# Performance work log

Measured on AMD Instinct MI355X. Metric: run time of the kernel, lower is better.

Reference implementation:

```python
import jax, jax.numpy as jnp
import numpy as np
import math

N_HEAD = 12

def alibi_slopes(h):
    x = (2 ** 8) ** (1.0 / h)
    return jnp.array([1.0 / x ** (i + 1) for i in range(h)], dtype=jnp.float32)

def setup_inputs() -> dict:
    key = jax.random.key(0)
    k0, k1, k2 = jax.random.split(key, 3)
    B, T, C = 4, 2048, 576
    x = jax.random.normal(k0, (B, T, C), dtype=jnp.float32)
    w_qkv = jax.random.normal(k1, (3 * C, C), dtype=jnp.float32) * 0.02
    w_proj = jax.random.normal(k2, (C, C), dtype=jnp.float32) * 0.02
    return {"x": x, "w_qkv": w_qkv, "w_proj": w_proj}

def reference(x, w_qkv, w_proj):
    B, T, C = x.shape
    H = N_HEAD
    D = C // H
    qkv = x @ w_qkv.T  # [B,T,3C]
    q, k, v = jnp.split(qkv, 3, axis=2)
    q = q.reshape(B, T, H, D).transpose(0, 2, 1, 3)  # [B,H,T,D]
    k = k.reshape(B, T, H, D).transpose(0, 2, 1, 3)
    v = v.reshape(B, T, H, D).transpose(0, 2, 1, 3)
    # value residual with v1=None: v = 0.5*v + 0.5*v = v (faithful no-op)
    scale = 1.0 / math.sqrt(D)
    att = jnp.einsum('bhid,bhjd->bhij', q, k) * scale  # [B,H,T,T]
    # ALiBi bias as written: (col - row).clamp(min=0) * slope (zero on causal part)
    col = jnp.arange(T, dtype=jnp.float32)[None, :]
    row = jnp.arange(T, dtype=jnp.float32)[:, None]
    bias = jnp.maximum(col - row, 0.0)[None, :, :] * alibi_slopes(H)[:, None, None]  # [H,T,T]
    att = att + bias[None]
    causal = (jnp.arange(T)[None, :] <= jnp.arange(T)[:, None])  # [T,T] lower-tri
    att = jnp.where(causal[None, None], att, -jnp.inf)
    att = jax.nn.softmax(att, axis=-1)
    y = jnp.einsum('bhij,bhjd->bhid', att, v)  # [B,H,T,D]
    y = y.transpose(0, 2, 1, 3).reshape(B, T, C)
    return y @ w_proj.T
```

## Files before the change

### kernel.cpp

```cpp
#include <hip/hip_runtime.h>
#include <math.h>

#define Bn 4
#define Tn 2048
#define Cn 576
#define Hn 12
#define Dn 48
#define Mn (Bn*Tn)
#define NPAD 1792

#define QSCALE (1.4426950408889634f * 0.14433756729740643f)

typedef short  short8  __attribute__((ext_vector_type(8)));
typedef float  floatx4 __attribute__((ext_vector_type(4)));
typedef unsigned short ushort_t;
typedef unsigned short ushort8_t __attribute__((ext_vector_type(8)));

static __device__ __forceinline__ unsigned short f2bf(float f) {
    union { float f; unsigned int u; } v; v.f = f;
    unsigned int r = v.u + 0x7FFFu + ((v.u >> 16) & 1u);
    return (unsigned short)(r >> 16);
}

static __device__ __forceinline__ unsigned int pack_trunc(float a, float b) {
    union { float f; unsigned int u; } ua, ub; ua.f = a; ub.f = b;
    return (ua.u >> 16) | (ub.u & 0xFFFF0000u);
}

static __device__ __forceinline__ void gload16(void* lds, const void* g) {
    __builtin_amdgcn_global_load_lds(
        (const __attribute__((address_space(1))) void*)g,
        (__attribute__((address_space(3))) void*)lds, 16, 0, 0);
}

template<int N> static __device__ __forceinline__ void vmgate() {
    if constexpr (N == 0)      asm volatile("s_waitcnt vmcnt(0)" ::: "memory");
    else if constexpr (N == 4) asm volatile("s_waitcnt vmcnt(4)" ::: "memory");
    else if constexpr (N == 8) asm volatile("s_waitcnt vmcnt(8)" ::: "memory");
}
static __device__ __forceinline__ void lgk0() {
    asm volatile("s_waitcnt lgkmcnt(0)" ::: "memory");
}
static __device__ __forceinline__ void barrier_fence() {
    asm volatile("" ::: "memory");
    __builtin_amdgcn_s_barrier();
    asm volatile("" ::: "memory");
}

template<int N> static __device__ __forceinline__ void wait_vm_lg() {
    if constexpr (N == 0)
        asm volatile("s_waitcnt vmcnt(0) lgkmcnt(0)" ::: "memory");
    else if constexpr (N == 3)
        asm volatile("s_waitcnt vmcnt(3) lgkmcnt(0)" ::: "memory");
    else if constexpr (N == 6)
        asm volatile("s_waitcnt vmcnt(6) lgkmcnt(0)" ::: "memory");
    else
        static_assert(N == -12345, "unsupported waitcnt immediate");
}

__global__ __launch_bounds__(256)
void cast3(const float* __restrict__ a, ushort_t* __restrict__ oa, int na4,
           const float* __restrict__ b, ushort_t* __restrict__ ob, int nb4,
           const float* __restrict__ c, ushort_t* __restrict__ oc, int nc4)
{
    int i = blockIdx.x * 256 + threadIdx.x;
    const float* src; ushort_t* dst; int idx;
    if (i < na4)                  { src = a; dst = oa; idx = i; }
    else if (i < na4 + nb4)       { src = b; dst = ob; idx = i - na4; }
    else if (i < na4 + nb4 + nc4) { src = c; dst = oc; idx = i - na4 - nb4; }
    else return;
    float4 v = ((const float4*)src)[idx];
    ushort4 o;
    o.x = f2bf(v.x); o.y = f2bf(v.y); o.z = f2bf(v.z); o.w = f2bf(v.w);
    ((ushort4*)dst)[idx] = o;
}

__global__ __launch_bounds__(512)
void gemm_qkv(const ushort_t* __restrict__ A, const ushort_t* __restrict__ W,
              ushort_t* __restrict__ outb)
{
    __shared__ __align__(16) ushort_t Ls[8][8192];

    const int tid  = threadIdx.x;
    const int wave = tid >> 6;
    const int lane = tid & 63;
    const int m    = lane & 15;
    const int g    = lane >> 4;
    const int wr   = wave >> 2;
    const int wn   = wave & 3;

    const int bid  = blockIdx.x;
    const int xcd  = bid & 7;
    const int slot = bid >> 3;
    const int ng   = slot % 7;
    const int mg   = xcd + 8 * (slot / 7);
    const int m0   = mg * 256;
    const int n0g  = ng * 256;

    const int srow = lane >> 2;
    const int schk = (lane & 3) * 16;
    const char* aS0 = (const char*)A + (size_t)(m0  + (wave*2+0)*16 + srow) * (Cn*2) + schk;
    const char* aS1 = (const char*)A + (size_t)(m0  + (wave*2+1)*16 + srow) * (Cn*2) + schk;
    const char* bS0 = (const char*)W + (size_t)(n0g + (wave*2+0)*16 + srow) * (Cn*2) + schk;
    const char* bS1 = (const char*)W + (size_t)(n0g + (wave*2+1)*16 + srow) * (Cn*2) + schk;

    const int aoff = (wr * 128 + m) * 64 + g * 16;
    const int boff = (wn * 64  + m) * 64 + g * 16;

    floatx4 acc[8][4];
    #pragma unroll
    for (int i = 0; i < 8; ++i)
        #pragma unroll
        for (int j = 0; j < 4; ++j)
            acc[i][j] = (floatx4){0.f, 0.f, 0.f, 0.f};

    short8 af[8], bf01[2], bf23[2];

    auto stageA = [&](int s) {
        gload16(&Ls[s][(wave*2+0)*512], aS0); aS0 += 64;
        gload16(&Ls[s][(wave*2+1)*512], aS1); aS1 += 64;
    };
    auto stageB = [&](int s) {
        gload16(&Ls[s][(wave*2+0)*512], bS0); bS0 += 64;
        gload16(&Ls[s][(wave*2+1)*512], bS1); bS1 += 64;
    };
    auto loadA = [&](int s) {
        const char* base = (const char*)&Ls[s][0] + aoff;
        #pragma unroll
        for (int mf = 0; mf < 8; ++mf) af[mf] = *(const short8*)(base + mf * 1024);
    };
    auto loadB = [&](int s, int nf0, short8 (&bf)[2]) {
        const char* base = (const char*)&Ls[s][0] + boff;
        bf[0] = *(const short8*)(base + (nf0 + 0) * 1024);
        bf[1] = *(const short8*)(base + (nf0 + 1) * 1024);
    };
    auto mfma16 = [&](short8 (&bf)[2], int nf0) {
        __builtin_amdgcn_s_setprio(1);
        #pragma unroll
        for (int mf = 0; mf < 8; ++mf) {
            acc[mf][nf0]     = __builtin_amdgcn_mfma_f32_16x16x32_bf16(af[mf], bf[0], acc[mf][nf0],     0, 0, 0);
            acc[mf][nf0 + 1] = __builtin_amdgcn_mfma_f32_16x16x32_bf16(af[mf], bf[1], acc[mf][nf0 + 1], 0, 0, 0);
        }
        __builtin_amdgcn_s_setprio(0);
    };

    stageA(0); stageB(1); stageA(2); stageB(3); stageA(4); stageB(5);
    vmgate<8>();
    barrier_fence();

    #define QKV_TILE(s0, d0, d1, d2, d3, G1m, G3m) do {                         \
        constexpr int A0 = (s0) & 7,      B0 = ((s0)+1) & 7;                    \
        constexpr int A1 = ((s0)+2) & 7,  B1 = ((s0)+3) & 7;                    \
        constexpr int S0 = ((s0)+6) & 7,  S1 = ((s0)+7) & 7;                    \
        constexpr int S2 = ((s0)+8) & 7,  S3 = ((s0)+9) & 7;                    \
                                                    \
        loadA(A0); loadB(B0, 0, bf01);                                          \
        if (d0) stageA(S0);                                                     \
        barrier_fence(); lgk0();                                                \
        mfma16(bf01, 0);                                                        \
        barrier_fence();                                                        \
                                                            \
        loadB(B0, 2, bf23);                                                     \
        if (d1) stageB(S1);                                                     \
        barrier_fence(); lgk0();                                                \
        mfma16(bf23, 2);                                                        \
        vmgate<G1m>();                                                          \
        barrier_fence();                                                        \
                                                    \
        loadA(A1); loadB(B1, 0, bf01);                                          \
        if (d2) stageA(S2);                                                     \
        barrier_fence(); lgk0();                                                \
        mfma16(bf01, 0);                                                        \
        barrier_fence();                                                        \
                                                            \
        loadB(B1, 2, bf23);                                                     \
        if (d3) stageB(S3);                                                     \
        barrier_fence(); lgk0();                                                \
        mfma16(bf23, 2);                                                        \
        vmgate<G3m>();                                                          \
        barrier_fence();                                                        \
    } while (0)

    #pragma unroll 1
    for (int tt = 0; tt < 3; ++tt) {
        QKV_TILE(0, 1, 1, 1, 1, 8, 8);
        QKV_TILE(4, 1, 1, 1, 1, 8, 8);
    }
    QKV_TILE(0, 1, 1, 1, 1, 8, 8);
    QKV_TILE(4, 1, 1, 0, 0, 8, 4);
    QKV_TILE(0, 0, 0, 0, 0, 0, -1);
    #undef QKV_TILE

    const size_t per = (size_t)Bn * Hn * Tn * Dn;
    const int b  = m0 >> 11;
    const int t0 = m0 & 2047;
    ushort_t* Lc = (ushort_t*)&Ls[0][0];

    #pragma unroll
    for (int h2 = 0; h2 < 2; ++h2) {
        const int  nbase = n0g + h2 * 128;
        const bool vmode = (nbase >= 1152);
        if ((wn >> 1) == h2) {
            if (!vmode) {
                #pragma unroll
                for (int mf = 0; mf < 8; ++mf)
                    #pragma unroll
                    for (int nf = 0; nf < 4; ++nf) {
                        const int  nfb = n0g + wn * 64 + nf * 16;
                        const float sc = (nfb < 576) ? QSCALE : 1.0f;
                        const int col = (wn & 1) * 64 + nf * 16 + m;
                        const int rb  = wr * 128 + mf * 16 + g * 4;
                        #pragma unroll
                        for (int r = 0; r < 4; ++r)
                            Lc[(rb + r) * 136 + col] = f2bf(acc[mf][nf][r] * sc);
                    }
            } else {
                #pragma unroll
                for (int mf = 0; mf < 8; ++mf)
                    #pragma unroll
                    for (int nf = 0; nf < 4; ++nf) {
                        const int col = (wn & 1) * 64 + nf * 16 + m;
                        const int rb  = wr * 128 + mf * 16 + g * 4;
                        ushort4 pk;
                        pk.x = f2bf(acc[mf][nf][0]); pk.y = f2bf(acc[mf][nf][1]);
                        pk.z = f2bf(acc[mf][nf][2]); pk.w = f2bf(acc[mf][nf][3]);
                        *(ushort4*)&Lc[col * 264 + rb] = pk;
                    }
            }
        }
        __syncthreads();
        if (!vmode) {
            #pragma unroll
            for (int it = 0; it < 8; ++it) {
                const int c   = tid + it * 512;
                const int row = c >> 4;
                const int c8  = (c & 15) * 8;
                const int n   = nbase + c8;
                const int which = (n >= 576);
                const int nn  = n - which * 576;
                const int h   = nn / 48, d = nn - h * 48;
                ushort_t* dst = outb + (size_t)which * per
                    + ((size_t)(b * Hn + h) * Tn + t0 + row) * Dn + d;
                *(ushort8_t*)dst = *(const ushort8_t*)&Lc[row * 136 + c8];
            }
        } else {
            #pragma unroll
            for (int it = 0; it < 8; ++it) {
                const int c   = tid + it * 512;
                const int col = c >> 5;
                const int rc  = (c & 31) * 8;
                const int n   = nbase + col;
                if (n < 1728) {
                    const int dd = n - 1152;
                    const int h  = dd / 48, d = dd - h * 48;
                    ushort_t* dst = outb + 2 * per
                        + ((size_t)(b * Hn + h) * Dn + d) * Tn + t0 + rc;
                    *(ushort8_t*)dst = *(const ushort8_t*)&Lc[col * 264 + rc];
                }
            }
        }
        __syncthreads();
    }
}

template<int MODE, int MTILE>
__global__ __launch_bounds__(256)
void gemm_mfma(const ushort_t* __restrict__ A, const ushort_t* __restrict__ W,
               ushort_t* __restrict__ outb, float* __restrict__ outf)
{
    constexpr int SA   = MTILE / 16;
    constexpr int NSEG = SA + 4;
    constexpr int PW   = NSEG / 4;
    constexpr int MF   = MTILE / 64;
    constexpr int NB   = 9;
    constexpr int NST  = Cn / 32;
    constexpr int AH   = 3;
    constexpr int NBUF = 4;
    __shared__ __align__(16) ushort_t Ls[NBUF][NSEG][512];

    const int tid  = threadIdx.x;
    const int wave = tid >> 6;
    const int lane = tid & 63;
    const int m    = lane & 15;
    const int g    = lane >> 4;
    const int bid  = blockIdx.x;
    const int xcd  = bid & 7;
    const int slot = bid >> 3;
    const int n0   = (slot % NB) * 64;
    const int m0   = (xcd + 8 * (slot / NB)) * MTILE;

    floatx4 acc[MF][4];
    #pragma unroll
    for (int i = 0; i < MF; ++i)
        #pragma unroll
        for (int j = 0; j < 4; ++j)
            acc[i][j] = (floatx4){0.f, 0.f, 0.f, 0.f};

    const char* gp[PW];
    int         si[PW];
    #pragma unroll
    for (int i = 0; i < PW; ++i) {
        int s = wave + i * 4;
        si[i] = s;
        gp[i] = (s < SA)
            ? (const char*)(A + (size_t)(m0 + s * 16 + m) * Cn + g * 8)
            : (const char*)(W + (size_t)(n0 + (s - SA) * 16 + m) * Cn + g * 8);
    }

    #pragma unroll
    for (int s = 0; s < AH; ++s)
        #pragma unroll
        for (int i = 0; i < PW; ++i) { gload16(&Ls[s][si[i]][0], gp[i]); gp[i] += 64; }
    wait_vm_lg<(AH - 1) * PW>();
    __builtin_amdgcn_s_barrier();

    for (int j = 0; j < NST; ++j) {
        if (j + AH < NST) {
            #pragma unroll
            for (int i = 0; i < PW; ++i) {
                gload16(&Ls[(j + AH) & (NBUF - 1)][si[i]][0], gp[i]);
                gp[i] += 64;
            }
        }
        const int buf = j & (NBUF - 1);
        short8 bf4[4];
        #pragma unroll
        for (int jj = 0; jj < 4; ++jj)
            bf4[jj] = *(const short8*)&Ls[buf][SA + jj][lane * 8];
        #pragma unroll
        for (int i = 0; i < MF; ++i) {
            short8 afr = *(const short8*)&Ls[buf][wave * MF + i][lane * 8];
            #pragma unroll
            for (int jj = 0; jj < 4; ++jj)
                acc[i][jj] = __builtin_amdgcn_mfma_f32_16x16x32_bf16(afr, bf4[jj], acc[i][jj], 0, 0, 0);
        }
        if (j < NST - AH)        wait_vm_lg<(AH - 1) * PW>();
        else if (j == NST - AH)  wait_vm_lg<(AH - 2) * PW>();
        else                     wait_vm_lg<0>();
        __builtin_amdgcn_s_barrier();
    }

    #pragma unroll
    for (int i = 0; i < MF; ++i) {
        #pragma unroll
        for (int r = 0; r < 4; ++r) {
            int mrow = m0 + wave * (MTILE / 4) + i * 16 + g * 4 + r;
            #pragma unroll
            for (int j = 0; j < 4; ++j)
                outf[(size_t)mrow * Cn + n0 + j * 16 + m] = acc[i][j][r];
        }
    }
}

__global__ __launch_bounds__(512, 6)
void attn_mfma(const ushort_t* __restrict__ Q, const ushort_t* __restrict__ K,
               const ushort_t* __restrict__ V, ushort_t* __restrict__ Y,
               const ushort_t* __restrict__ zb)
{
    __shared__ __align__(16) ushort_t QPs[16][512];
    __shared__ __align__(16) ushort_t Ks[2][8][512];
    __shared__ __align__(16) ushort_t Vs[2][6][512];

    const int id   = blockIdx.x;
    const int kk   = id / 48;
    const int bh   = id - kk * 48;
    const int QT   = (kk & 1) ? (kk >> 1) : (15 - (kk >> 1));
    const int tid  = threadIdx.x;
    const int wave = tid >> 6;
    const int lane = tid & 63;
    const int m    = lane & 15;
    const int g    = lane >> 4;
    const int q0   = QT * 128;
    const int nkt  = 2 * QT + 2;

    const ushort_t* Qp = Q + (size_t)bh * Tn * Dn;
    const ushort_t* Kp = K + (size_t)bh * Tn * Dn;
    const ushort_t* Vp = V + (size_t)bh * Dn * Tn;

    {
        const char* qrp = (const char*)(Qp + (size_t)(q0 + wave * 16 + m) * Dn);
        gload16(&QPs[wave * 2 + 0][0], qrp + g * 16);
        gload16(&QPs[wave * 2 + 1][0], (g < 2) ? (qrp + 64 + g * 16) : (const char*)zb);
    }

    const bool  kpad = ((wave & 1) == 1) && (g >= 2);
    const char* kptr = kpad ? (const char*)zb
        : (const char*)(Kp + (size_t)((wave >> 1) * 16 + m) * Dn) + (wave & 1) * 64 + g * 16;
    const int   kadv = kpad ? 0 : 64 * Dn * 2;
    const char* vptr = (const char*)(Vp + (size_t)((wave >> 1) * 16 + m) * Tn)
                       + (wave & 1) * 64 + g * 16;
    const int   vadv = 64 * 2;

    gload16(&Ks[0][wave][0], kptr); kptr += kadv;
    if (wave < 6) { gload16(&Vs[0][wave][0], vptr); vptr += vadv; }
    __syncthreads();

    short8 bq[2];
    bq[0] = *(const short8*)&QPs[wave * 2 + 0][lane * 8];
    bq[1] = *(const short8*)&QPs[wave * 2 + 1][lane * 8];

    floatx4 acc[3];
    #pragma unroll
    for (int t = 0; t < 3; ++t) acc[t] = (floatx4){0.f, 0.f, 0.f, 0.f};
    float l_tot = 0.f;
    const int qrow  = q0 + wave * 16 + m;
    const int qwmin = q0 + wave * 16;
    const int qwmax = qwmin + 15;

    for (int jt = 0; jt < nkt; ++jt) {
        const int cur = jt & 1;
        const int j0  = jt * 64;
        if (jt + 1 < nkt) {
            gload16(&Ks[cur ^ 1][wave][0], kptr); kptr += kadv;
            if (wave < 6) { gload16(&Vs[cur ^ 1][wave][0], vptr); vptr += vadv; }
        }

        if (j0 <= qwmax) {
            floatx4 s[4];
            #pragma unroll
            for (int t = 0; t < 4; ++t) {
                s[t] = (floatx4){0.f, 0.f, 0.f, 0.f};
                #pragma unroll
                for (int kc = 0; kc < 2; ++kc) {
                    short8 ak = *(const short8*)&Ks[cur][t * 2 + kc][lane * 8];
                    s[t] = __builtin_amdgcn_mfma_f32_16x16x32_bf16(ak, bq[kc], s[t], 0, 0, 0);
                }
            }

            float p[4][4];
            float lsum = 0.f;
            if (j0 + 63 > qwmin) {
                #pragma unroll
                for (int t = 0; t < 4; ++t)
                    #pragma unroll
                    for (int r = 0; r < 4; ++r) {
                        int j = j0 + t * 16 + g * 4 + r;
                        float v = (j <= qrow) ? s[t][r] : -1e30f;
                        float e = __builtin_amdgcn_exp2f(v);
                        p[t][r] = e; lsum += e;
                    }
            } else {
                #pragma unroll
                for (int t = 0; t < 4; ++t)
                    #pragma unroll
                    for (int r = 0; r < 4; ++r) {
                        float e = __builtin_amdgcn_exp2f(s[t][r]);
                        p[t][r] = e; lsum += e;
                    }
            }
            lsum += __shfl_xor(lsum, 16);
            lsum += __shfl_xor(lsum, 32);
            l_tot += lsum;

            #pragma unroll
            for (int t = 0; t < 4; ++t) {
                uint2 w2;
                w2.x = pack_trunc(p[t][0], p[t][1]);
                w2.y = pack_trunc(p[t][2], p[t][3]);
                *(uint2*)&QPs[wave * 2 + (t >> 1)]
                             [(2 * (t & 1) + (g >> 1)) * 128 + m * 8 + (g & 1) * 4] = w2;
            }
            asm volatile("s_waitcnt lgkmcnt(0)" ::: "memory");

            #pragma unroll
            for (int kc = 0; kc < 2; ++kc) {
                short8 bp = *(const short8*)&QPs[wave * 2 + kc][lane * 8];
                #pragma unroll
                for (int t = 0; t < 3; ++t) {
                    short8 av = *(const short8*)&Vs[cur][t * 2 + kc][lane * 8];
                    acc[t] = __builtin_amdgcn_mfma_f32_16x16x32_bf16(av, bp, acc[t], 0, 0, 0);
                }
            }
        }

        __syncthreads();
    }

    const float inv = 1.0f / l_tot;
    const int b = bh / Hn;
    const int h = bh - b * Hn;
    ushort_t* yp = Y + ((size_t)(b * Tn + qrow)) * Cn + h * Dn;
    #pragma unroll
    for (int t = 0; t < 3; ++t) {
        ushort4 o;
        o.x = f2bf(acc[t][0] * inv);
        o.y = f2bf(acc[t][1] * inv);
        o.z = f2bf(acc[t][2] * inv);
        o.w = f2bf(acc[t][3] * inv);
        *(ushort4*)&yp[t * 16 + g * 4] = o;
    }
}

extern "C" void kernel_launch(void* const* d_in, const int* in_sizes, int n_in,
                              void* d_out, int out_size, void* d_ws, size_t ws_size,
                              hipStream_t stream)
{
    const float* x      = (const float*)d_in[0];
    const float* w_qkv  = (const float*)d_in[1];
    const float* w_proj = (const float*)d_in[2];
    float* out = (float*)d_out;

    const size_t per = (size_t)Bn * Hn * Tn * Dn;

    ushort_t* xb  = (ushort_t*)d_ws;
    ushort_t* wqb = xb  + (size_t)Mn * Cn;
    ushort_t* wpb = wqb + (size_t)3 * Cn * Cn;
    ushort_t* qkv = wpb + (size_t)Cn * Cn;
    ushort_t* yb  = qkv + 3 * per;
    ushort_t* zb  = yb  + (size_t)Mn * Cn;

    hipMemsetAsync(zb, 0, 256, stream);

    const int na4 = Mn * Cn / 4, nb4 = 3 * Cn * Cn / 4, nc4 = Cn * Cn / 4;
    cast3<<<dim3((na4 + nb4 + nc4 + 255) / 256), dim3(256), 0, stream>>>(
        x, xb, na4, w_qkv, wqb, nb4, w_proj, wpb, nc4);

    gemm_qkv<<<dim3(224), dim3(512), 0, stream>>>(xb, wqb, qkv);

    attn_mfma<<<dim3((Tn / 128) * Bn * Hn), dim3(512), 0, stream>>>(
        qkv, qkv + per, qkv + 2 * per, yb, zb);

    gemm_mfma<1, 128><<<dim3((Mn / 128) * 9), dim3(256), 0, stream>>>(yb, wpb, nullptr, out);
}
```

Measured before the change: 163.4 us.

## Double attention KV tile to 128 keys and fold zero-buffer memset into cast kernel

The attention kernel now processes 128 keys per iteration instead of 64. This halves the loop trip count and the number of block-wide syncs, and the score tile is reused in place for the probabilities. The K/V shared-memory buffers double in size, so the occupancy hint drops from 6 to 4 blocks per CU. Separately, the hipMemsetAsync that zeroed the padding buffer is removed and the zeroing is done inside the cast kernel, saving one launch. The larger tile raises register and LDS use, and the diagonal tile now does more masked work.

```diff
diff --git a/kernel.cpp b/kernel.cpp
--- a/kernel.cpp
+++ b/kernel.cpp
@@ -7,7 +7,6 @@
 #define Hn 12
 #define Dn 48
 #define Mn (Bn*Tn)
-#define NPAD 1792
 
 #define QSCALE (1.4426950408889634f * 0.14433756729740643f)
 
@@ -61,9 +60,14 @@
 __global__ __launch_bounds__(256)
 void cast3(const float* __restrict__ a, ushort_t* __restrict__ oa, int na4,
            const float* __restrict__ b, ushort_t* __restrict__ ob, int nb4,
-           const float* __restrict__ c, ushort_t* __restrict__ oc, int nc4)
+           const float* __restrict__ c, ushort_t* __restrict__ oc, int nc4,
+           ushort_t* __restrict__ zb)
 {
     int i = blockIdx.x * 256 + threadIdx.x;
+    if (blockIdx.x == 0 && threadIdx.x < 16) {
+        float4 z = (float4){0.f, 0.f, 0.f, 0.f};
+        ((float4*)zb)[threadIdx.x] = z;
+    }
     const float* src; ushort_t* dst; int idx;
     if (i < na4)                  { src = a; dst = oa; idx = i; }
     else if (i < na4 + nb4)       { src = b; dst = ob; idx = i - na4; }
@@ -153,26 +157,22 @@
         constexpr int A1 = ((s0)+2) & 7,  B1 = ((s0)+3) & 7;                    \
         constexpr int S0 = ((s0)+6) & 7,  S1 = ((s0)+7) & 7;                    \
         constexpr int S2 = ((s0)+8) & 7,  S3 = ((s0)+9) & 7;                    \
-                                                    \
         loadA(A0); loadB(B0, 0, bf01);                                          \
         if (d0) stageA(S0);                                                     \
         barrier_fence(); lgk0();                                                \
         mfma16(bf01, 0);                                                        \
         barrier_fence();                                                        \
-                                                            \
         loadB(B0, 2, bf23);                                                     \
         if (d1) stageB(S1);                                                     \
         barrier_fence(); lgk0();                                                \
         mfma16(bf23, 2);                                                        \
         vmgate<G1m>();                                                          \
         barrier_fence();                                                        \
-                                                    \
         loadA(A1); loadB(B1, 0, bf01);                                          \
         if (d2) stageA(S2);                                                     \
         barrier_fence(); lgk0();                                                \
         mfma16(bf01, 0);                                                        \
         barrier_fence();                                                        \
-                                                            \
         loadB(B1, 2, bf23);                                                     \
         if (d3) stageB(S3);                                                     \
         barrier_fence(); lgk0();                                                \
@@ -352,14 +352,14 @@
     }
 }
 
-__global__ __launch_bounds__(512, 6)
+__global__ __launch_bounds__(512, 4)
 void attn_mfma(const ushort_t* __restrict__ Q, const ushort_t* __restrict__ K,
                const ushort_t* __restrict__ V, ushort_t* __restrict__ Y,
                const ushort_t* __restrict__ zb)
 {
     __shared__ __align__(16) ushort_t QPs[16][512];
-    __shared__ __align__(16) ushort_t Ks[2][8][512];
-    __shared__ __align__(16) ushort_t Vs[2][6][512];
+    __shared__ __align__(16) ushort_t Ks[2][16][512];
+    __shared__ __align__(16) ushort_t Vs[2][12][512];
 
     const int id   = blockIdx.x;
     const int kk   = id / 48;
@@ -371,7 +371,7 @@
     const int m    = lane & 15;
     const int g    = lane >> 4;
     const int q0   = QT * 128;
-    const int nkt  = 2 * QT + 2;
+    const int nkt  = QT + 1;
 
     const ushort_t* Qp = Q + (size_t)bh * Tn * Dn;
     const ushort_t* Kp = K + (size_t)bh * Tn * Dn;
@@ -383,16 +383,24 @@
         gload16(&QPs[wave * 2 + 1][0], (g < 2) ? (qrp + 64 + g * 16) : (const char*)zb);
     }
 
-    const bool  kpad = ((wave & 1) == 1) && (g >= 2);
-    const char* kptr = kpad ? (const char*)zb
+    const bool  kpad  = ((wave & 1) == 1) && (g >= 2);
+    const char* kptrA = kpad ? (const char*)zb
         : (const char*)(Kp + (size_t)((wave >> 1) * 16 + m) * Dn) + (wave & 1) * 64 + g * 16;
-    const int   kadv = kpad ? 0 : 64 * Dn * 2;
-    const char* vptr = (const char*)(Vp + (size_t)((wave >> 1) * 16 + m) * Tn)
-                       + (wave & 1) * 64 + g * 16;
-    const int   vadv = 64 * 2;
-
-    gload16(&Ks[0][wave][0], kptr); kptr += kadv;
-    if (wave < 6) { gload16(&Vs[0][wave][0], vptr); vptr += vadv; }
+    const char* kptrB = kpad ? (const char*)zb
+        : kptrA + 64 * Dn * 2;
+    const int   kadv  = kpad ? 0 : 128 * Dn * 2;
+
+    const char* vptr0 = (const char*)(Vp + (size_t)((wave >> 1) * 16 + m) * Tn)
+                        + (2 * (wave & 1)) * 64 + g * 16;
+    const char* vptr1 = vptr0 + 64;
+    const int   vadv  = 128 * 2;
+
+    gload16(&Ks[0][wave][0],     kptrA); kptrA += kadv;
+    gload16(&Ks[0][wave + 8][0], kptrB); kptrB += kadv;
+    if (wave < 6) {
+        gload16(&Vs[0][2 * wave + 0][0], vptr0); vptr0 += vadv;
+        gload16(&Vs[0][2 * wave + 1][0], vptr1); vptr1 += vadv;
+    }
     __syncthreads();
 
     short8 bq[2];
@@ -404,21 +412,24 @@
     for (int t = 0; t < 3; ++t) acc[t] = (floatx4){0.f, 0.f, 0.f, 0.f};
     float l_tot = 0.f;
     const int qrow  = q0 + wave * 16 + m;
-    const int qwmin = q0 + wave * 16;
-    const int qwmax = qwmin + 15;
+    const int qwmax = q0 + wave * 16 + 15;
 
     for (int jt = 0; jt < nkt; ++jt) {
         const int cur = jt & 1;
-        const int j0  = jt * 64;
+        const int j0  = jt * 128;
         if (jt + 1 < nkt) {
-            gload16(&Ks[cur ^ 1][wave][0], kptr); kptr += kadv;
-            if (wave < 6) { gload16(&Vs[cur ^ 1][wave][0], vptr); vptr += vadv; }
+            gload16(&Ks[cur ^ 1][wave][0],     kptrA); kptrA += kadv;
+            gload16(&Ks[cur ^ 1][wave + 8][0], kptrB); kptrB += kadv;
+            if (wave < 6) {
+                gload16(&Vs[cur ^ 1][2 * wave + 0][0], vptr0); vptr0 += vadv;
+                gload16(&Vs[cur ^ 1][2 * wave + 1][0], vptr1); vptr1 += vadv;
+            }
         }
 
         if (j0 <= qwmax) {
-            floatx4 s[4];
-            #pragma unroll
-            for (int t = 0; t < 4; ++t) {
+            floatx4 s[8];
+            #pragma unroll
+            for (int t = 0; t < 8; ++t) {
                 s[t] = (floatx4){0.f, 0.f, 0.f, 0.f};
                 #pragma unroll
                 for (int kc = 0; kc < 2; ++kc) {
@@ -427,25 +438,24 @@
                 }
             }
 
-            float p[4][4];
             float lsum = 0.f;
-            if (j0 + 63 > qwmin) {
-                #pragma unroll
-                for (int t = 0; t < 4; ++t)
+            if (jt == nkt - 1) {
+                #pragma unroll
+                for (int t = 0; t < 8; ++t)
                     #pragma unroll
                     for (int r = 0; r < 4; ++r) {
                         int j = j0 + t * 16 + g * 4 + r;
                         float v = (j <= qrow) ? s[t][r] : -1e30f;
                         float e = __builtin_amdgcn_exp2f(v);
-                        p[t][r] = e; lsum += e;
+                        s[t][r] = e; lsum += e;
                     }
             } else {
                 #pragma unroll
-                for (int t = 0; t < 4; ++t)
+                for (int t = 0; t < 8; ++t)
                     #pragma unroll
                     for (int r = 0; r < 4; ++r) {
                         float e = __builtin_amdgcn_exp2f(s[t][r]);
-                        p[t][r] = e; lsum += e;
+                        s[t][r] = e; lsum += e;
                     }
             }
             lsum += __shfl_xor(lsum, 16);
@@ -453,22 +463,27 @@
             l_tot += lsum;
 
             #pragma unroll
-            for (int t = 0; t < 4; ++t) {
-                uint2 w2;
-                w2.x = pack_trunc(p[t][0], p[t][1]);
-                w2.y = pack_trunc(p[t][2], p[t][3]);
-                *(uint2*)&QPs[wave * 2 + (t >> 1)]
-                             [(2 * (t & 1) + (g >> 1)) * 128 + m * 8 + (g & 1) * 4] = w2;
-            }
-            asm volatile("s_waitcnt lgkmcnt(0)" ::: "memory");
-
-            #pragma unroll
-            for (int kc = 0; kc < 2; ++kc) {
-                short8 bp = *(const short8*)&QPs[wave * 2 + kc][lane * 8];
-                #pragma unroll
-                for (int t = 0; t < 3; ++t) {
-                    short8 av = *(const short8*)&Vs[cur][t * 2 + kc][lane * 8];
-                    acc[t] = __builtin_amdgcn_mfma_f32_16x16x32_bf16(av, bp, acc[t], 0, 0, 0);
+            for (int hh = 0; hh < 2; ++hh) {
+                #pragma unroll
+                for (int t4 = 0; t4 < 4; ++t4) {
+                    const int t = hh * 4 + t4;
+                    uint2 w2;
+                    w2.x = pack_trunc(s[t][0], s[t][1]);
+                    w2.y = pack_trunc(s[t][2], s[t][3]);
+                    *(uint2*)&QPs[wave * 2 + (t4 >> 1)]
+                                 [(2 * (t4 & 1) + (g >> 1)) * 128 + m * 8 + (g & 1) * 4] = w2;
+                }
+                asm volatile("s_waitcnt lgkmcnt(0)" ::: "memory");
+
+                #pragma unroll
+                for (int kc2 = 0; kc2 < 2; ++kc2) {
+                    const int kcq = hh * 2 + kc2;
+                    short8 bp = *(const short8*)&QPs[wave * 2 + kc2][lane * 8];
+                    #pragma unroll
+                    for (int t = 0; t < 3; ++t) {
+                        short8 av = *(const short8*)&Vs[cur][t * 4 + kcq][lane * 8];
+                        acc[t] = __builtin_amdgcn_mfma_f32_16x16x32_bf16(av, bp, acc[t], 0, 0, 0);
+                    }
                 }
             }
         }
@@ -509,11 +524,9 @@
     ushort_t* yb  = qkv + 3 * per;
     ushort_t* zb  = yb  + (size_t)Mn * Cn;
 
-    hipMemsetAsync(zb, 0, 256, stream);
-
     const int na4 = Mn * Cn / 4, nb4 = 3 * Cn * Cn / 4, nc4 = Cn * Cn / 4;
     cast3<<<dim3((na4 + nb4 + nc4 + 255) / 256), dim3(256), 0, stream>>>(
-        x, xb, na4, w_qkv, wqb, nb4, w_proj, wpb, nc4);
+        x, xb, na4, w_qkv, wqb, nb4, w_proj, wpb, nc4, zb);
 
     gemm_qkv<<<dim3(224), dim3(512), 0, stream>>>(xb, wqb, qkv);
 
```

Result: slower. 166.9 us (+2.1%).

## Compact attention K/V shared tiles, raise occupancy, fold zero-buffer memset into cast

Applied to the files above, without the earlier changes.

The attention kernel's shared buffers are merged into one array. K tiles are now loaded as contiguous row-major 64x48 blocks (6 waves) instead of padded 64-wide fragments, and A operands are read with a per-lane row offset. This shrinks LDS per block, and launch bounds go from 6 to 8 blocks per CU to allow more resident blocks. The separate hipMemsetAsync for the zero buffer is removed and done inside the cast kernel, saving one launch. The risks are register pressure from the higher occupancy target, and the strided K reads may now cause LDS bank conflicts.

```diff
diff --git a/kernel.cpp b/kernel.cpp
--- a/kernel.cpp
+++ b/kernel.cpp
@@ -7,7 +7,6 @@
 #define Hn 12
 #define Dn 48
 #define Mn (Bn*Tn)
-#define NPAD 1792
 
 #define QSCALE (1.4426950408889634f * 0.14433756729740643f)
 
@@ -61,9 +60,14 @@
 __global__ __launch_bounds__(256)
 void cast3(const float* __restrict__ a, ushort_t* __restrict__ oa, int na4,
            const float* __restrict__ b, ushort_t* __restrict__ ob, int nb4,
-           const float* __restrict__ c, ushort_t* __restrict__ oc, int nc4)
+           const float* __restrict__ c, ushort_t* __restrict__ oc, int nc4,
+           ushort_t* __restrict__ zb)
 {
     int i = blockIdx.x * 256 + threadIdx.x;
+    if (blockIdx.x == 0 && threadIdx.x < 16) {
+        float4 z = (float4){0.f, 0.f, 0.f, 0.f};
+        ((float4*)zb)[threadIdx.x] = z;
+    }
     const float* src; ushort_t* dst; int idx;
     if (i < na4)                  { src = a; dst = oa; idx = i; }
     else if (i < na4 + nb4)       { src = b; dst = ob; idx = i - na4; }
@@ -153,26 +157,22 @@
         constexpr int A1 = ((s0)+2) & 7,  B1 = ((s0)+3) & 7;                    \
         constexpr int S0 = ((s0)+6) & 7,  S1 = ((s0)+7) & 7;                    \
         constexpr int S2 = ((s0)+8) & 7,  S3 = ((s0)+9) & 7;                    \
-                                                    \
         loadA(A0); loadB(B0, 0, bf01);                                          \
         if (d0) stageA(S0);                                                     \
         barrier_fence(); lgk0();                                                \
         mfma16(bf01, 0);                                                        \
         barrier_fence();                                                        \
-                                                            \
         loadB(B0, 2, bf23);                                                     \
         if (d1) stageB(S1);                                                     \
         barrier_fence(); lgk0();                                                \
         mfma16(bf23, 2);                                                        \
         vmgate<G1m>();                                                          \
         barrier_fence();                                                        \
-                                                    \
         loadA(A1); loadB(B1, 0, bf01);                                          \
         if (d2) stageA(S2);                                                     \
         barrier_fence(); lgk0();                                                \
         mfma16(bf01, 0);                                                        \
         barrier_fence();                                                        \
-                                                            \
         loadB(B1, 2, bf23);                                                     \
         if (d3) stageB(S3);                                                     \
         barrier_fence(); lgk0();                                                \
@@ -352,14 +352,12 @@
     }
 }
 
-__global__ __launch_bounds__(512, 6)
+__global__ __launch_bounds__(512, 8)
 void attn_mfma(const ushort_t* __restrict__ Q, const ushort_t* __restrict__ K,
                const ushort_t* __restrict__ V, ushort_t* __restrict__ Y,
                const ushort_t* __restrict__ zb)
 {
-    __shared__ __align__(16) ushort_t QPs[16][512];
-    __shared__ __align__(16) ushort_t Ks[2][8][512];
-    __shared__ __align__(16) ushort_t Vs[2][6][512];
+    __shared__ __align__(16) ushort_t SMEM[20480];
 
     const int id   = blockIdx.x;
     const int kk   = id / 48;
@@ -379,25 +377,28 @@
 
     {
         const char* qrp = (const char*)(Qp + (size_t)(q0 + wave * 16 + m) * Dn);
-        gload16(&QPs[wave * 2 + 0][0], qrp + g * 16);
-        gload16(&QPs[wave * 2 + 1][0], (g < 2) ? (qrp + 64 + g * 16) : (const char*)zb);
-    }
-
-    const bool  kpad = ((wave & 1) == 1) && (g >= 2);
-    const char* kptr = kpad ? (const char*)zb
-        : (const char*)(Kp + (size_t)((wave >> 1) * 16 + m) * Dn) + (wave & 1) * 64 + g * 16;
-    const int   kadv = kpad ? 0 : 64 * Dn * 2;
-    const char* vptr = (const char*)(Vp + (size_t)((wave >> 1) * 16 + m) * Tn)
-                       + (wave & 1) * 64 + g * 16;
-    const int   vadv = 64 * 2;
-
-    gload16(&Ks[0][wave][0], kptr); kptr += kadv;
-    if (wave < 6) { gload16(&Vs[0][wave][0], vptr); vptr += vadv; }
+        gload16(&SMEM[(wave * 2 + 0) * 512], qrp + g * 16);
+        gload16(&SMEM[(wave * 2 + 1) * 512], (g < 2) ? (qrp + 64 + g * 16) : (const char*)zb);
+    }
+
+    const char* kptr = (const char*)Kp + wave * 1024 + lane * 16;
+    const int   vseg = wave - 2;
+    const char* vptr = (const char*)(Vp + (size_t)((vseg >> 1) * 16 + m) * Tn)
+                       + (vseg & 1) * 64 + g * 16;
+
+    if (tid == 0) {
+        ushort8_t z = (ushort8_t){0, 0, 0, 0, 0, 0, 0, 0};
+        *(ushort8_t*)&SMEM[11264] = z;
+        *(ushort8_t*)&SMEM[11272] = z;
+    }
+
+    if (wave < 6)  { gload16(&SMEM[8192 + wave * 512],  kptr); kptr += 6144; }
+    if (wave >= 2) { gload16(&SMEM[14336 + vseg * 512], vptr); vptr += 128; }
     __syncthreads();
 
     short8 bq[2];
-    bq[0] = *(const short8*)&QPs[wave * 2 + 0][lane * 8];
-    bq[1] = *(const short8*)&QPs[wave * 2 + 1][lane * 8];
+    bq[0] = *(const short8*)&SMEM[(wave * 2 + 0) * 512 + lane * 8];
+    bq[1] = *(const short8*)&SMEM[(wave * 2 + 1) * 512 + lane * 8];
 
     floatx4 acc[3];
     #pragma unroll
@@ -406,23 +407,25 @@
     const int qrow  = q0 + wave * 16 + m;
     const int qwmin = q0 + wave * 16;
     const int qwmax = qwmin + 15;
+    const int koff  = m * 48 + g * 8;
 
     for (int jt = 0; jt < nkt; ++jt) {
         const int cur = jt & 1;
         const int j0  = jt * 64;
         if (jt + 1 < nkt) {
-            gload16(&Ks[cur ^ 1][wave][0], kptr); kptr += kadv;
-            if (wave < 6) { gload16(&Vs[cur ^ 1][wave][0], vptr); vptr += vadv; }
+            if (wave < 6)  { gload16(&SMEM[8192 + (cur ^ 1) * 3072 + wave * 512],  kptr); kptr += 6144; }
+            if (wave >= 2) { gload16(&SMEM[14336 + (cur ^ 1) * 3072 + vseg * 512], vptr); vptr += 128; }
         }
 
         if (j0 <= qwmax) {
+            const ushort_t* Kb = &SMEM[8192 + cur * 3072 + koff];
             floatx4 s[4];
             #pragma unroll
             for (int t = 0; t < 4; ++t) {
                 s[t] = (floatx4){0.f, 0.f, 0.f, 0.f};
                 #pragma unroll
                 for (int kc = 0; kc < 2; ++kc) {
-                    short8 ak = *(const short8*)&Ks[cur][t * 2 + kc][lane * 8];
+                    short8 ak = *(const short8*)(Kb + t * 768 + kc * 32);
                     s[t] = __builtin_amdgcn_mfma_f32_16x16x32_bf16(ak, bq[kc], s[t], 0, 0, 0);
                 }
             }
@@ -457,17 +460,17 @@
                 uint2 w2;
                 w2.x = pack_trunc(p[t][0], p[t][1]);
                 w2.y = pack_trunc(p[t][2], p[t][3]);
-                *(uint2*)&QPs[wave * 2 + (t >> 1)]
-                             [(2 * (t & 1) + (g >> 1)) * 128 + m * 8 + (g & 1) * 4] = w2;
+                *(uint2*)&SMEM[(wave * 2 + (t >> 1)) * 512
+                               + (2 * (t & 1) + (g >> 1)) * 128 + m * 8 + (g & 1) * 4] = w2;
             }
             asm volatile("s_waitcnt lgkmcnt(0)" ::: "memory");
 
             #pragma unroll
             for (int kc = 0; kc < 2; ++kc) {
-                short8 bp = *(const short8*)&QPs[wave * 2 + kc][lane * 8];
+                short8 bp = *(const short8*)&SMEM[(wave * 2 + kc) * 512 + lane * 8];
                 #pragma unroll
                 for (int t = 0; t < 3; ++t) {
-                    short8 av = *(const short8*)&Vs[cur][t * 2 + kc][lane * 8];
+                    short8 av = *(const short8*)&SMEM[14336 + cur * 3072 + (t * 2 + kc) * 512 + lane * 8];
                     acc[t] = __builtin_amdgcn_mfma_f32_16x16x32_bf16(av, bp, acc[t], 0, 0, 0);
                 }
             }
@@ -509,11 +512,9 @@
     ushort_t* yb  = qkv + 3 * per;
     ushort_t* zb  = yb  + (size_t)Mn * Cn;
 
-    hipMemsetAsync(zb, 0, 256, stream);
-
     const int na4 = Mn * Cn / 4, nb4 = 3 * Cn * Cn / 4, nc4 = Cn * Cn / 4;
     cast3<<<dim3((na4 + nb4 + nc4 + 255) / 256), dim3(256), 0, stream>>>(
-        x, xb, na4, w_qkv, wqb, nb4, w_proj, wpb, nc4);
+        x, xb, na4, w_qkv, wqb, nb4, w_proj, wpb, nc4, zb);
 
     gemm_qkv<<<dim3(224), dim3(512), 0, stream>>>(xb, wqb, qkv);
 
```

Result: slower. 189.6 us (+16.0%).
